# Performance work log

Measured on AMD Instinct MI355X. Metric: run time of the kernel, lower is better.

The kernel has to match this reference:

```python
import jax, jax.numpy as jnp
import numpy as np

NUM_GRAPHS = 1024

def setup_inputs() -> dict:
    key = jax.random.key(0)
    k1, k2 = jax.random.split(key)
    x = jax.random.normal(k1, (1000000, 256), dtype=jnp.float32)
    batch = jnp.sort(jax.random.randint(k2, (1000000,), 0, NUM_GRAPHS, dtype=jnp.int64))
    return {"x": x, "batch": batch}

def reference(x, batch):
    # global_mean_pool: per-segment sum over node features, normalized by count.
    sums = jax.ops.segment_sum(x, batch, num_segments=NUM_GRAPHS)  # [G, F]
    counts = jax.ops.segment_sum(jnp.ones((x.shape[0],), dtype=x.dtype), batch,
                                 num_segments=NUM_GRAPHS)  # [G]
    counts = jnp.maximum(counts, 1.0)  # avoid div-by-zero for empty segments
    return sums / counts[:, None]
```

## Files before the change

kernel.cpp:

```cpp
#include <hip/hip_runtime.h>


__device__ __forceinline__ float4 f4add(float4 a, float4 b) {
    return make_float4(a.x + b.x, a.y + b.y, a.z + b.z, a.w + b.w);
}

__global__ __launch_bounds__(256) void meanpool_kernel(
    const float* __restrict__ x,
    const int* __restrict__ batch,
    float* __restrict__ out,
    int N)
{
    const int g = blockIdx.x;

    __shared__ int s_b[2];
    if (threadIdx.x < 2) {
        const int target = g + (int)threadIdx.x;
        int lo = 0, hi = N;
        while (lo < hi) {
            int mid = (lo + hi) >> 1;
            if (batch[mid] < target) lo = mid + 1; else hi = mid;
        }
        s_b[threadIdx.x] = lo;
    }
    __syncthreads();
    const int start = s_b[0];
    const int end   = s_b[1];
    const int count = end - start;

    const int q = threadIdx.x & 63;
    const int r = threadIdx.x >> 6;
    const float4* __restrict__ xv = reinterpret_cast<const float4*>(x);

    float4 a0 = make_float4(0.f, 0.f, 0.f, 0.f);
    float4 a1 = a0, a2 = a0, a3 = a0;

    int i = start + r;
    for (; i + 12 < end; i += 16) {
        a0 = f4add(a0, xv[(size_t)(i     ) * 64 + q]);
        a1 = f4add(a1, xv[(size_t)(i +  4) * 64 + q]);
        a2 = f4add(a2, xv[(size_t)(i +  8) * 64 + q]);
        a3 = f4add(a3, xv[(size_t)(i + 12) * 64 + q]);
    }
    for (; i < end; i += 4) {
        a0 = f4add(a0, xv[(size_t)i * 64 + q]);
    }
    a0 = f4add(f4add(a0, a1), f4add(a2, a3));

    __shared__ float4 s_part[3][64];
    if (r > 0) s_part[r - 1][q] = a0;
    __syncthreads();
    if (r == 0) {
        a0 = f4add(a0, s_part[0][q]);
        a0 = f4add(a0, s_part[1][q]);
        a0 = f4add(a0, s_part[2][q]);
        const float inv = 1.0f / (float)(count > 1 ? count : 1);
        float4* __restrict__ outv = reinterpret_cast<float4*>(out);
        outv[(size_t)g * 64 + q] =
            make_float4(a0.x * inv, a0.y * inv, a0.z * inv, a0.w * inv);
    }
}

extern "C" void kernel_launch(void* const* d_in, const int* in_sizes, int n_in,
                              void* d_out, int out_size, void* d_ws, size_t ws_size,
                              hipStream_t stream) {
    const float* x     = (const float*)d_in[0];
    const int*   batch = (const int*)d_in[1];
    float*       out   = (float*)d_out;
    const int N = in_sizes[1];
    const int G = out_size / 256;

    meanpool_kernel<<<G, 256, 0, stream>>>(x, batch, out, N);
}
```

Before: 184.0 us.

## Split segment mean pool into chunked atomic accumulation plus normalize pass

Replaces the one-block-per-graph kernel with a node-chunked kernel. Each wavefront sums 32 contiguous rows and flushes per-segment partial sums and counts to the output with float atomics. A second kernel then divides by the counts, and the output and count buffers are zeroed with memsets first. The aim is to spread the 1GB read evenly over about 7800 blocks rather than 1024 segment-sized blocks. The cost is roughly 256 atomics per segment boundary per wavefront, two extra memsets and an extra launch, and float atomics make the summation order nondeterministic.

Result: slower. 232.6 us (+26.4%).

```diff
diff --git a/kernel.cpp b/kernel.cpp
--- a/kernel.cpp
+++ b/kernel.cpp
@@ -1,64 +1,87 @@
 #include <hip/hip_runtime.h>
 
+
+#define CHUNK 128
+#define TCH   32
 
 __device__ __forceinline__ float4 f4add(float4 a, float4 b) {
     return make_float4(a.x + b.x, a.y + b.y, a.z + b.z, a.w + b.w);
 }
 
-__global__ __launch_bounds__(256) void meanpool_kernel(
+__device__ __forceinline__ void atomAddF(float* p, float v) {
+    __hip_atomic_fetch_add(p, v, __ATOMIC_RELAXED, __HIP_MEMORY_SCOPE_AGENT);
+}
+
+__device__ __forceinline__ void flush_seg(float* __restrict__ out,
+                                          int* __restrict__ cnt,
+                                          int g, int q, float4 a, int len) {
+    float* p = out + (size_t)g * 256 + q * 4;
+    atomAddF(p + 0, a.x);
+    atomAddF(p + 1, a.y);
+    atomAddF(p + 2, a.z);
+    atomAddF(p + 3, a.w);
+    if (q == 0) atomicAdd(cnt + g, len);
+}
+
+__global__ __launch_bounds__(256) void meanpool_phase1(
     const float* __restrict__ x,
     const int* __restrict__ batch,
     float* __restrict__ out,
+    int* __restrict__ cnt,
     int N)
 {
-    const int g = blockIdx.x;
-
-    __shared__ int s_b[2];
-    if (threadIdx.x < 2) {
-        const int target = g + (int)threadIdx.x;
-        int lo = 0, hi = N;
-        while (lo < hi) {
-            int mid = (lo + hi) >> 1;
-            if (batch[mid] < target) lo = mid + 1; else hi = mid;
-        }
-        s_b[threadIdx.x] = lo;
-    }
-    __syncthreads();
-    const int start = s_b[0];
-    const int end   = s_b[1];
-    const int count = end - start;
-
     const int q = threadIdx.x & 63;
     const int r = threadIdx.x >> 6;
+
+    int i = blockIdx.x * CHUNK + r * TCH;
+    if (i >= N) return;
+    const int e = min(N, i + TCH);
+
     const float4* __restrict__ xv = reinterpret_cast<const float4*>(x);
 
-    float4 a0 = make_float4(0.f, 0.f, 0.f, 0.f);
-    float4 a1 = a0, a2 = a0, a3 = a0;
+    float4 acc = make_float4(0.f, 0.f, 0.f, 0.f);
+    int cg = batch[i];
+    int segStart = i;
 
-    int i = start + r;
-    for (; i + 12 < end; i += 16) {
-        a0 = f4add(a0, xv[(size_t)(i     ) * 64 + q]);
-        a1 = f4add(a1, xv[(size_t)(i +  4) * 64 + q]);
-        a2 = f4add(a2, xv[(size_t)(i +  8) * 64 + q]);
-        a3 = f4add(a3, xv[(size_t)(i + 12) * 64 + q]);
+    while (i < e) {
+        if (i + 4 <= e) {
+            const int b0 = batch[i], b1 = batch[i + 1];
+            const int b2 = batch[i + 2], b3 = batch[i + 3];
+            if (b0 == cg && b1 == cg && b2 == cg && b3 == cg) {
+                float4 v0 = xv[(size_t)(i    ) * 64 + q];
+                float4 v1 = xv[(size_t)(i + 1) * 64 + q];
+                float4 v2 = xv[(size_t)(i + 2) * 64 + q];
+                float4 v3 = xv[(size_t)(i + 3) * 64 + q];
+                acc = f4add(acc, f4add(f4add(v0, v1), f4add(v2, v3)));
+                i += 4;
+                continue;
+            }
+        }
+        const int b = batch[i];
+        if (b != cg) {
+            flush_seg(out, cnt, cg, q, acc, i - segStart);
+            acc = make_float4(0.f, 0.f, 0.f, 0.f);
+            cg = b;
+            segStart = i;
+        }
+        acc = f4add(acc, xv[(size_t)i * 64 + q]);
+        ++i;
     }
-    for (; i < end; i += 4) {
-        a0 = f4add(a0, xv[(size_t)i * 64 + q]);
-    }
-    a0 = f4add(f4add(a0, a1), f4add(a2, a3));
+    flush_seg(out, cnt, cg, q, acc, i - segStart);
+}
 
-    __shared__ float4 s_part[3][64];
-    if (r > 0) s_part[r - 1][q] = a0;
-    __syncthreads();
-    if (r == 0) {
-        a0 = f4add(a0, s_part[0][q]);
-        a0 = f4add(a0, s_part[1][q]);
-        a0 = f4add(a0, s_part[2][q]);
-        const float inv = 1.0f / (float)(count > 1 ? count : 1);
-        float4* __restrict__ outv = reinterpret_cast<float4*>(out);
-        outv[(size_t)g * 64 + q] =
-            make_float4(a0.x * inv, a0.y * inv, a0.z * inv, a0.w * inv);
-    }
+__global__ __launch_bounds__(64) void meanpool_phase2(
+    float* __restrict__ out,
+    const int* __restrict__ cnt)
+{
+    const int g = blockIdx.x;
+    const int q = threadIdx.x;
+    const int c = cnt[g];
+    const float inv = 1.0f / (float)(c > 1 ? c : 1);
+    float4* ov = reinterpret_cast<float4*>(out);
+    float4 v = ov[(size_t)g * 64 + q];
+    ov[(size_t)g * 64 + q] =
+        make_float4(v.x * inv, v.y * inv, v.z * inv, v.w * inv);
 }
 
 extern "C" void kernel_launch(void* const* d_in, const int* in_sizes, int n_in,
@@ -67,8 +90,15 @@
     const float* x     = (const float*)d_in[0];
     const int*   batch = (const int*)d_in[1];
     float*       out   = (float*)d_out;
+    int*         cnt   = (int*)d_ws;
+
     const int N = in_sizes[1];
     const int G = out_size / 256;
+    const int NB = (N + CHUNK - 1) / CHUNK;
 
-    meanpool_kernel<<<G, 256, 0, stream>>>(x, batch, out, N);
+    hipMemsetAsync(out, 0, (size_t)out_size * sizeof(float), stream);
+    hipMemsetAsync(cnt, 0, (size_t)G * sizeof(int), stream);
+
+    meanpool_phase1<<<NB, 256, 0, stream>>>(x, batch, out, cnt, N);
+    meanpool_phase2<<<G, 64, 0, stream>>>(out, cnt);
 }
```

## Split segment mean-pool into fixed row chunks with atomic accumulation and normalize pass

Applied to the files above, without the earlier changes.

Replaces one-block-per-graph with one block per 512-row chunk that finds segment boundaries in shared memory, reduces each segment piece, and atomically adds partial sums and counts into the output. A second kernel divides by the counts. This is meant to balance work across more blocks and improve memory-level parallelism, at the cost of float atomics, two memsets, an extra launch, and nondeterministic summation order.

New measurement: 194.8 us. +5.9%, slower.

```diff
diff --git a/kernel.cpp b/kernel.cpp
--- a/kernel.cpp
+++ b/kernel.cpp
@@ -1,64 +1,122 @@
 #include <hip/hip_runtime.h>
 
+
+#define CHUNK 512
+#define MAXB  16
 
 __device__ __forceinline__ float4 f4add(float4 a, float4 b) {
     return make_float4(a.x + b.x, a.y + b.y, a.z + b.z, a.w + b.w);
 }
 
-__global__ __launch_bounds__(256) void meanpool_kernel(
+__device__ __forceinline__ void atomAddF(float* p, float v) {
+    __hip_atomic_fetch_add(p, v, __ATOMIC_RELAXED, __HIP_MEMORY_SCOPE_AGENT);
+}
+
+__global__ __launch_bounds__(256, 8) void meanpool_phase1(
     const float* __restrict__ x,
     const int* __restrict__ batch,
     float* __restrict__ out,
+    int* __restrict__ cnt,
     int N)
 {
-    const int g = blockIdx.x;
+    const int tid = threadIdx.x;
+    const int q = tid & 63;
+    const int r = tid >> 6;
+    const int B = blockIdx.x * CHUNK;
+    const int E = min(N, B + CHUNK);
+    const int L = E - B;
 
-    __shared__ int s_b[2];
-    if (threadIdx.x < 2) {
-        const int target = g + (int)threadIdx.x;
-        int lo = 0, hi = N;
-        while (lo < hi) {
-            int mid = (lo + hi) >> 1;
-            if (batch[mid] < target) lo = mid + 1; else hi = mid;
+    __shared__ int    s_batch[CHUNK];
+    __shared__ int    s_nb;
+    __shared__ int    s_bpos[MAXB];
+    __shared__ float4 s_part[3][64];
+
+    for (int p = tid; p < L; p += 256) s_batch[p] = batch[B + p];
+    if (tid == 0) s_nb = 0;
+    __syncthreads();
+
+    for (int p = tid; p < L; p += 256) {
+        bool bd = (p == 0) || (s_batch[p] != s_batch[p - 1]);
+        if (bd) {
+            int k = atomicAdd(&s_nb, 1);
+            if (k < MAXB) s_bpos[k] = p;
         }
-        s_b[threadIdx.x] = lo;
     }
     __syncthreads();
-    const int start = s_b[0];
-    const int end   = s_b[1];
-    const int count = end - start;
+    const int nb = s_nb;
 
-    const int q = threadIdx.x & 63;
-    const int r = threadIdx.x >> 6;
     const float4* __restrict__ xv = reinterpret_cast<const float4*>(x);
 
-    float4 a0 = make_float4(0.f, 0.f, 0.f, 0.f);
-    float4 a1 = a0, a2 = a0, a3 = a0;
+    if (nb <= MAXB) {
+        if (tid == 0 && nb > 1) {
+            for (int a = 1; a < nb; ++a) {
+                int v = s_bpos[a]; int b = a - 1;
+                while (b >= 0 && s_bpos[b] > v) { s_bpos[b + 1] = s_bpos[b]; --b; }
+                s_bpos[b + 1] = v;
+            }
+        }
+        __syncthreads();
 
-    int i = start + r;
-    for (; i + 12 < end; i += 16) {
-        a0 = f4add(a0, xv[(size_t)(i     ) * 64 + q]);
-        a1 = f4add(a1, xv[(size_t)(i +  4) * 64 + q]);
-        a2 = f4add(a2, xv[(size_t)(i +  8) * 64 + q]);
-        a3 = f4add(a3, xv[(size_t)(i + 12) * 64 + q]);
+        for (int k = 0; k < nb; ++k) {
+            const int s = B + s_bpos[k];
+            const int e = (k + 1 < nb) ? (B + s_bpos[k + 1]) : E;
+            const int g = s_batch[s - B];
+
+            float4 a0 = make_float4(0.f, 0.f, 0.f, 0.f);
+            float4 a1 = a0, a2 = a0, a3 = a0;
+            int i = s + r;
+            for (; i + 12 < e; i += 16) {
+                a0 = f4add(a0, xv[(size_t)(i     ) * 64 + q]);
+                a1 = f4add(a1, xv[(size_t)(i +  4) * 64 + q]);
+                a2 = f4add(a2, xv[(size_t)(i +  8) * 64 + q]);
+                a3 = f4add(a3, xv[(size_t)(i + 12) * 64 + q]);
+            }
+            for (; i < e; i += 4) a0 = f4add(a0, xv[(size_t)i * 64 + q]);
+            a0 = f4add(f4add(a0, a1), f4add(a2, a3));
+
+            if (r > 0) s_part[r - 1][q] = a0;
+            __syncthreads();
+            if (r == 0) {
+                a0 = f4add(a0, s_part[0][q]);
+                a0 = f4add(a0, s_part[1][q]);
+                a0 = f4add(a0, s_part[2][q]);
+                float* p = out + (size_t)g * 256 + q * 4;
+                atomAddF(p + 0, a0.x);
+                atomAddF(p + 1, a0.y);
+                atomAddF(p + 2, a0.z);
+                atomAddF(p + 3, a0.w);
+                if (q == 0) atomicAdd(cnt + g, e - s);
+            }
+            __syncthreads();
+        }
+    } else {
+        if (r == 0) {
+            for (int i = B; i < E; ++i) {
+                const int g = s_batch[i - B];
+                float4 v = xv[(size_t)i * 64 + q];
+                float* p = out + (size_t)g * 256 + q * 4;
+                atomAddF(p + 0, v.x);
+                atomAddF(p + 1, v.y);
+                atomAddF(p + 2, v.z);
+                atomAddF(p + 3, v.w);
+                if (q == 0) atomicAdd(cnt + g, 1);
+            }
+        }
     }
-    for (; i < end; i += 4) {
-        a0 = f4add(a0, xv[(size_t)i * 64 + q]);
-    }
-    a0 = f4add(f4add(a0, a1), f4add(a2, a3));
+}
 
-    __shared__ float4 s_part[3][64];
-    if (r > 0) s_part[r - 1][q] = a0;
-    __syncthreads();
-    if (r == 0) {
-        a0 = f4add(a0, s_part[0][q]);
-        a0 = f4add(a0, s_part[1][q]);
-        a0 = f4add(a0, s_part[2][q]);
-        const float inv = 1.0f / (float)(count > 1 ? count : 1);
-        float4* __restrict__ outv = reinterpret_cast<float4*>(out);
-        outv[(size_t)g * 64 + q] =
-            make_float4(a0.x * inv, a0.y * inv, a0.z * inv, a0.w * inv);
-    }
+__global__ __launch_bounds__(64) void meanpool_phase2(
+    float* __restrict__ out,
+    const int* __restrict__ cnt)
+{
+    const int g = blockIdx.x;
+    const int q = threadIdx.x;
+    const int c = cnt[g];
+    const float inv = 1.0f / (float)(c > 1 ? c : 1);
+    float4* ov = reinterpret_cast<float4*>(out);
+    float4 v = ov[(size_t)g * 64 + q];
+    ov[(size_t)g * 64 + q] =
+        make_float4(v.x * inv, v.y * inv, v.z * inv, v.w * inv);
 }
 
 extern "C" void kernel_launch(void* const* d_in, const int* in_sizes, int n_in,
@@ -67,8 +125,15 @@
     const float* x     = (const float*)d_in[0];
     const int*   batch = (const int*)d_in[1];
     float*       out   = (float*)d_out;
+    int*         cnt   = (int*)d_ws;
+
     const int N = in_sizes[1];
     const int G = out_size / 256;
+    const int NB = (N + CHUNK - 1) / CHUNK;
 
-    meanpool_kernel<<<G, 256, 0, stream>>>(x, batch, out, N);
+    hipMemsetAsync(out, 0, (size_t)out_size * sizeof(float), stream);
+    hipMemsetAsync(cnt, 0, (size_t)G * sizeof(int), stream);
+
+    meanpool_phase1<<<NB, 256, 0, stream>>>(x, batch, out, cnt, N);
+    meanpool_phase2<<<G, 64, 0, stream>>>(out, cnt);
 }
```

## Split each segment across four blocks with separate bounds and combine kernels

Applied to the files above, without the earlier changes.

Segment boundaries are now computed once by a dedicated binary-search kernel. Each segment's rows are split into quarters summed by four blocks, giving 4096 blocks instead of 1024 to raise occupancy and memory-level parallelism on the 1 GB streaming read. A third small kernel adds the four partials and divides by the count. This adds two extra launches and a workspace round trip, and falls back to the old kernel if the workspace is too small.

New measurement: 192.7 us. +4.8%, slower.

```diff
diff --git a/kernel.cpp b/kernel.cpp
--- a/kernel.cpp
+++ b/kernel.cpp
@@ -5,14 +5,80 @@
     return make_float4(a.x + b.x, a.y + b.y, a.z + b.z, a.w + b.w);
 }
 
-__global__ __launch_bounds__(256) void meanpool_kernel(
-    const float* __restrict__ x,
-    const int* __restrict__ batch,
-    float* __restrict__ out,
-    int N)
+__global__ __launch_bounds__(256) void bounds_kernel(
+    const int* __restrict__ batch, int* __restrict__ bounds, int N, int G)
+{
+    const int g = blockIdx.x * 256 + threadIdx.x;
+    if (g > G) return;
+    int lo = 0, hi = N;
+    while (lo < hi) {
+        int mid = (lo + hi) >> 1;
+        if (batch[mid] < g) lo = mid + 1; else hi = mid;
+    }
+    bounds[g] = lo;
+}
+
+__global__ __launch_bounds__(256) void quarter_sum_kernel(
+    const float* __restrict__ x, const int* __restrict__ bounds,
+    float* __restrict__ partial)
+{
+    const int g  = blockIdx.x >> 2;
+    const int qt = blockIdx.x & 3;
+    const int s0 = bounds[g];
+    const int e0 = bounds[g + 1];
+    const int len = e0 - s0;
+    const int qs = s0 + (int)(((long long)len * qt)       >> 2);
+    const int qe = s0 + (int)(((long long)len * (qt + 1)) >> 2);
+
+    const int q = threadIdx.x & 63;
+    const int r = threadIdx.x >> 6;
+    const float4* __restrict__ xv = reinterpret_cast<const float4*>(x);
+
+    float4 a0 = make_float4(0.f, 0.f, 0.f, 0.f);
+    float4 a1 = a0, a2 = a0, a3 = a0;
+    int i = qs + r;
+    for (; i + 12 < qe; i += 16) {
+        a0 = f4add(a0, xv[(size_t)(i     ) * 64 + q]);
+        a1 = f4add(a1, xv[(size_t)(i +  4) * 64 + q]);
+        a2 = f4add(a2, xv[(size_t)(i +  8) * 64 + q]);
+        a3 = f4add(a3, xv[(size_t)(i + 12) * 64 + q]);
+    }
+    for (; i < qe; i += 4) a0 = f4add(a0, xv[(size_t)i * 64 + q]);
+    a0 = f4add(f4add(a0, a1), f4add(a2, a3));
+
+    __shared__ float4 s_part[3][64];
+    if (r > 0) s_part[r - 1][q] = a0;
+    __syncthreads();
+    if (r == 0) {
+        a0 = f4add(a0, s_part[0][q]);
+        a0 = f4add(a0, s_part[1][q]);
+        a0 = f4add(a0, s_part[2][q]);
+        reinterpret_cast<float4*>(partial)[(size_t)blockIdx.x * 64 + q] = a0;
+    }
+}
+
+__global__ __launch_bounds__(64) void combine_kernel(
+    const float* __restrict__ partial, const int* __restrict__ bounds,
+    float* __restrict__ out)
 {
     const int g = blockIdx.x;
+    const int q = threadIdx.x;
+    const float4* __restrict__ pv = reinterpret_cast<const float4*>(partial);
+    float4 a =        pv[(size_t)(4 * g    ) * 64 + q];
+    a = f4add(a,      pv[(size_t)(4 * g + 1) * 64 + q]);
+    a = f4add(a,      pv[(size_t)(4 * g + 2) * 64 + q]);
+    a = f4add(a,      pv[(size_t)(4 * g + 3) * 64 + q]);
+    const int len = bounds[g + 1] - bounds[g];
+    const float inv = 1.0f / (float)(len > 1 ? len : 1);
+    reinterpret_cast<float4*>(out)[(size_t)g * 64 + q] =
+        make_float4(a.x * inv, a.y * inv, a.z * inv, a.w * inv);
+}
 
+__global__ __launch_bounds__(256) void meanpool_v1(
+    const float* __restrict__ x, const int* __restrict__ batch,
+    float* __restrict__ out, int N)
+{
+    const int g = blockIdx.x;
     __shared__ int s_b[2];
     if (threadIdx.x < 2) {
         const int target = g + (int)threadIdx.x;
@@ -34,7 +100,6 @@
 
     float4 a0 = make_float4(0.f, 0.f, 0.f, 0.f);
     float4 a1 = a0, a2 = a0, a3 = a0;
-
     int i = start + r;
     for (; i + 12 < end; i += 16) {
         a0 = f4add(a0, xv[(size_t)(i     ) * 64 + q]);
@@ -42,9 +107,7 @@
         a2 = f4add(a2, xv[(size_t)(i +  8) * 64 + q]);
         a3 = f4add(a3, xv[(size_t)(i + 12) * 64 + q]);
     }
-    for (; i < end; i += 4) {
-        a0 = f4add(a0, xv[(size_t)i * 64 + q]);
-    }
+    for (; i < end; i += 4) a0 = f4add(a0, xv[(size_t)i * 64 + q]);
     a0 = f4add(f4add(a0, a1), f4add(a2, a3));
 
     __shared__ float4 s_part[3][64];
@@ -55,8 +118,7 @@
         a0 = f4add(a0, s_part[1][q]);
         a0 = f4add(a0, s_part[2][q]);
         const float inv = 1.0f / (float)(count > 1 ? count : 1);
-        float4* __restrict__ outv = reinterpret_cast<float4*>(out);
-        outv[(size_t)g * 64 + q] =
+        reinterpret_cast<float4*>(out)[(size_t)g * 64 + q] =
             make_float4(a0.x * inv, a0.y * inv, a0.z * inv, a0.w * inv);
     }
 }
@@ -67,8 +129,21 @@
     const float* x     = (const float*)d_in[0];
     const int*   batch = (const int*)d_in[1];
     float*       out   = (float*)d_out;
+
     const int N = in_sizes[1];
     const int G = out_size / 256;
 
-    meanpool_kernel<<<G, 256, 0, stream>>>(x, batch, out, N);
+    const size_t partial_bytes = (size_t)G * 4 * 256 * sizeof(float);
+    const size_t bounds_bytes  = (size_t)(G + 1) * sizeof(int);
+    if (ws_size < partial_bytes + bounds_bytes) {
+        meanpool_v1<<<G, 256, 0, stream>>>(x, batch, out, N);
+        return;
+    }
+
+    float* partial = (float*)d_ws;
+    int*   bounds  = (int*)((char*)d_ws + partial_bytes);
+
+    bounds_kernel<<<(G + 256) / 256, 256, 0, stream>>>(batch, bounds, N, G);
+    quarter_sum_kernel<<<G * 4, 256, 0, stream>>>(x, bounds, partial);
+    combine_kernel<<<G, 64, 0, stream>>>(partial, bounds, out);
 }
```
